# Kernel tuning notes

Hardware: AMD Instinct MI355X
Metric: run time of the kernel (lower is better)

## Reference

```python
import jax, jax.numpy as jnp
import numpy as np

ALPHA = 0.2   # leaky relu negative slope
NEG_INF = -1e12


def setup_inputs() -> dict:
    key = jax.random.key(0)
    k1, k2, k3, k4 = jax.random.split(key, 4)
    B, N, H = 8, 2048, 128
    inp = jax.random.normal(k1, (B, N, H), dtype=jnp.float32)
    A = (jax.random.uniform(k2, (B, N, N)) < 0.05).astype(jnp.float32)
    # xavier_uniform with gain 1.414
    gain = 1.414
    limW = gain * np.sqrt(6.0 / (H + H))
    W = jax.random.uniform(k3, (H, H), minval=-limW, maxval=limW, dtype=jnp.float32)
    lima = gain * np.sqrt(6.0 / (2 * H + 1))
    a = jax.random.uniform(k4, (2 * H, 1), minval=-lima, maxval=lima, dtype=jnp.float32)
    return {"inp": inp, "A": A, "W": W, "a": a}


def reference(inp, A, W, a):
    B, N, H = inp.shape
    Wh = jnp.matmul(inp, W)                      # [B,N,H]
    Wh1 = jnp.matmul(Wh, a[:H, :])               # [B,N,1]
    Wh2 = jnp.matmul(Wh, a[H:, :])               # [B,N,1]
    A_ = A + jnp.eye(N, dtype=A.dtype)           # add self loops
    e = (Wh1 + jnp.swapaxes(Wh2, 1, 2)) * A_     # [B,N,N]
    e = jnp.where(e >= 0, e, ALPHA * e)          # leaky relu
    scores = jnp.where(A_ > 0, e, NEG_INF)
    attention = jax.nn.softmax(scores, axis=2)   # dropout: eval mode -> identity
    h_prime = jnp.matmul(attention, Wh)          # [B,N,H]
    return jax.nn.elu(h_prime)                   # concat=True branch
```

## Files before the change

kernel.cpp:

```cpp
#include <hip/hip_runtime.h>
#include <hip/hip_bf16.h>
#include <math.h>

typedef __attribute__((ext_vector_type(4))) float f32x4;
typedef __attribute__((ext_vector_type(8))) short s16x8;

constexpr int Nc = 2048;
constexpr int Hc = 128;
constexpr int ROWS = 8 * 2048;

__device__ __forceinline__ unsigned short f2bf(float f) {
  unsigned u = __float_as_uint(f);
  return (unsigned short)((u + 0x7fffu + ((u >> 16) & 1u)) >> 16);
}
__device__ __forceinline__ float bf2f(unsigned short b) {
  return __uint_as_float(((unsigned)b) << 16);
}

typedef __attribute__((address_space(3))) unsigned u32_lds;
typedef __attribute__((address_space(1))) const unsigned u32_glb;
__device__ __forceinline__ void stage16(const void* g, void* l) {
  __builtin_amdgcn_global_load_lds((u32_glb*)g, (u32_lds*)l, 16, 0, 0);
}

__global__ void prep_kernel(const float* __restrict__ W,
                            unsigned short* __restrict__ Wt_hi,
                            unsigned short* __restrict__ Wt_lo) {
  const int id = blockIdx.x * 256 + threadIdx.x;
  const int k = id >> 7, h = id & 127;
  const float w = W[id];
  const unsigned short hi = f2bf(w);
  const unsigned short lo = f2bf(w - bf2f(hi));
  const int off = ((k >> 3) * 128 + h) * 8 + (k & 7);
  Wt_hi[off] = hi;
  Wt_lo[off] = lo;
}

__global__ __launch_bounds__(256) void whmfma_kernel(
    const float* __restrict__ inp, const unsigned short* __restrict__ Wt_hi,
    const unsigned short* __restrict__ Wt_lo, const float* __restrict__ a,
    unsigned short* __restrict__ Vsw, float* __restrict__ Wh1,
    float* __restrict__ Wh2) {
  const int t = threadIdx.x, w_ = t >> 6, l = t & 63;
  const int lrow = l & 15, kq = l >> 4;
  const int r0 = blockIdx.x * 64 + w_ * 16;
  const int row = r0 + lrow;

  s16x8 ahi[4], alo[4];
#pragma unroll
  for (int ks = 0; ks < 4; ++ks) {
    const float* xp = inp + (size_t)row * 128 + ks * 32 + kq * 8;
    const f32x4 x0 = *(const f32x4*)xp;
    const f32x4 x1 = *(const f32x4*)(xp + 4);
    s16x8 th, tl;
#pragma unroll
    for (int e = 0; e < 4; ++e) {
      const unsigned short b0 = f2bf(x0[e]), b1 = f2bf(x1[e]);
      th[e] = (short)b0;       tl[e] = (short)f2bf(x0[e] - bf2f(b0));
      th[4 + e] = (short)b1;   tl[4 + e] = (short)f2bf(x1[e] - bf2f(b1));
    }
    ahi[ks] = th; alo[ks] = tl;
  }

  f32x4 acc[8];
#pragma unroll
  for (int nb = 0; nb < 8; ++nb) acc[nb] = (f32x4){0.f, 0.f, 0.f, 0.f};

#pragma unroll
  for (int ks = 0; ks < 4; ++ks) {
#pragma unroll
    for (int nb = 0; nb < 8; ++nb) {
      const size_t bo = ((size_t)(ks * 4 + kq) * 128 + nb * 16 + lrow) * 8;
      const s16x8 bh = *(const s16x8*)(Wt_hi + bo);
      const s16x8 bl = *(const s16x8*)(Wt_lo + bo);
      acc[nb] = __builtin_amdgcn_mfma_f32_16x16x32_bf16(ahi[ks], bh, acc[nb], 0, 0, 0);
      acc[nb] = __builtin_amdgcn_mfma_f32_16x16x32_bf16(alo[ks], bh, acc[nb], 0, 0, 0);
      acc[nb] = __builtin_amdgcn_mfma_f32_16x16x32_bf16(ahi[ks], bl, acc[nb], 0, 0, 0);
    }
  }

  float a1v[8], a2v[8];
#pragma unroll
  for (int nb = 0; nb < 8; ++nb) {
    a1v[nb] = a[nb * 16 + lrow];
    a2v[nb] = a[128 + nb * 16 + lrow];
  }
#pragma unroll
  for (int rg = 0; rg < 4; ++rg) {
    float p1 = 0.f, p2 = 0.f;
#pragma unroll
    for (int nb = 0; nb < 8; ++nb) {
      p1 = fmaf(acc[nb][rg], a1v[nb], p1);
      p2 = fmaf(acc[nb][rg], a2v[nb], p2);
    }
#pragma unroll
    for (int off = 1; off < 16; off <<= 1) {
      p1 += __shfl_xor(p1, off);
      p2 += __shfl_xor(p2, off);
    }
    if (lrow == 0) {
      const int node = r0 + kq * 4 + rg;
      Wh1[node] = p1;
      Wh2[node] = p2;
    }
  }

  const int b = r0 >> 11, jt = (r0 >> 6) & 31;
  unsigned short* __restrict__ vbase = Vsw + (size_t)(b * 32 + jt) * (8 * 128 * 8);
  const int nl0 = w_ * 16 + kq * 4;
  const int jg = nl0 >> 3, j0 = nl0 & 7;
#pragma unroll
  for (int nb = 0; nb < 8; ++nb) {
    unsigned q0, q1;
    asm("v_cvt_pk_bf16_f32 %0, %1, %2" : "=v"(q0) : "v"(acc[nb][0]), "v"(acc[nb][1]));
    asm("v_cvt_pk_bf16_f32 %0, %1, %2" : "=v"(q1) : "v"(acc[nb][2]), "v"(acc[nb][3]));
    *(uint2*)(vbase + ((size_t)jg * 128 + nb * 16 + lrow) * 8 + j0) = make_uint2(q0, q1);
  }
}

__global__ __launch_bounds__(256, 3) void attn_kernel(
    const float* __restrict__ A, const unsigned short* __restrict__ Vsw,
    const float* __restrict__ Wh1, const float* __restrict__ Wh2,
    float* __restrict__ out) {
  __shared__ union {
    struct { float Ab[2][16][256]; float w2[2][256]; } st;
    struct { float m[64]; float l[64]; float invl[16]; float a4[4][16][132]; } mg;
  } sm;

  const int t = threadIdx.x, w_ = t >> 6, l = t & 63;
  const int lrow = l & 15, lq = l >> 4, g8 = lq * 8;
  const int bid = (blockIdx.x & 7) * 128 + (blockIdx.x >> 3);
  const int b = bid >> 7;
  const int irow = (bid & 127) * 16 + lrow;

  const float* __restrict__ Abase = A + (size_t)bid * 16 * 2048;
  const float* __restrict__ Wh2b = Wh2 + (size_t)b * 2048;
  const float wh1r = Wh1[(size_t)bid * 16 + lrow];
  const unsigned short* __restrict__ Vb = Vsw + (size_t)b * (32 * 8 * 128 * 8);
  const size_t vlane = (size_t)(lq * 128 + lrow) * 8;

#pragma unroll
  for (int rr = 0; rr < 4; ++rr) {
    const int r = w_ * 4 + rr;
    stage16(Abase + (size_t)r * 2048 + ((l ^ (r & 7)) << 2), &sm.st.Ab[0][r][0]);
  }
  if (w_ == 0) stage16(Wh2b + l * 4, &sm.st.w2[0][0]);

  f32x4 acc[8];
#pragma unroll
  for (int nb = 0; nb < 8; ++nb) acc[nb] = (f32x4){0.f, 0.f, 0.f, 0.f};
  float m = -1e30f, lsum = 0.f;

  for (int c = 0; c < 8; ++c) {
    __syncthreads();
    const int buf = c & 1;
    if (c < 7) {
#pragma unroll
      for (int rr = 0; rr < 4; ++rr) {
        const int r = w_ * 4 + rr;
        stage16(Abase + (size_t)r * 2048 + (c + 1) * 256 + ((l ^ (r & 7)) << 2),
                &sm.st.Ab[buf ^ 1][r][0]);
      }
      if (w_ == 0) stage16(Wh2b + (c + 1) * 256 + l * 4, &sm.st.w2[buf ^ 1][0]);
    }

    const int jb_loc = w_ * 64;
    const int jb_glob = c * 256 + jb_loc;
    const unsigned short* __restrict__ Vt = Vb + (size_t)(c * 4 + w_) * (8 * 128 * 8);

    s16x8 v0[4], v1[4];
#pragma unroll
    for (int nb = 0; nb < 4; ++nb) {
      v0[nb] = *(const s16x8*)(Vt + vlane + nb * 128);
      v1[nb] = *(const s16x8*)(Vt + vlane + 4096 + nb * 128);
    }

    f32x4 av[4], wv[4];
    const int c0 = (jb_loc + g8) >> 2;
#pragma unroll
    for (int q = 0; q < 4; ++q) {
      const int cq = c0 + (q & 1) + (q >> 1) * 8;
      av[q] = *(const f32x4*)&sm.st.Ab[buf][lrow][(cq ^ (lrow & 7)) << 2];
      wv[q] = *(const f32x4*)&sm.st.w2[buf][jb_loc + g8 + (q & 1) * 4 + (q >> 1) * 32];
    }

    float s[16];
    float tm = -3e30f;
#pragma unroll
    for (int idx = 0; idx < 16; ++idx) {
      const int j = jb_glob + (idx >> 3) * 32 + g8 + (idx & 7);
      const float aval = av[idx >> 2][idx & 3];
      const float raw = wh1r + wv[idx >> 2][idx & 3];
      const float lr = fmaxf(raw, 0.2f * raw);
      const float mult = aval + ((j == irow) ? 1.f : 0.f);
      const float sv = (mult > 0.f) ? mult * lr : -2e30f;
      s[idx] = sv;
      tm = fmaxf(tm, sv);
    }
    tm = fmaxf(tm, __shfl_xor(tm, 16));
    tm = fmaxf(tm, __shfl_xor(tm, 32));
    const float mnew = (tm > m + 8.f) ? tm : m;
    if (__ballot(mnew != m)) {
      const float alpha = __expf(m - mnew);
      lsum *= alpha;
      const int rb4 = lq * 4;
      const float a0 = __shfl(alpha, rb4);
      const float a1 = __shfl(alpha, rb4 + 1);
      const float a2 = __shfl(alpha, rb4 + 2);
      const float a3 = __shfl(alpha, rb4 + 3);
#pragma unroll
      for (int nb = 0; nb < 8; ++nb) {
        acc[nb][0] *= a0; acc[nb][1] *= a1; acc[nb][2] *= a2; acc[nb][3] *= a3;
      }
      m = mnew;
    }

    float p[16];
    float tsum = 0.f;
#pragma unroll
    for (int idx = 0; idx < 16; ++idx) {
      p[idx] = __expf(s[idx] - m);
      tsum += p[idx];
    }
    tsum += __shfl_xor(tsum, 16);
    tsum += __shfl_xor(tsum, 32);
    lsum += tsum;

    union { unsigned u[4]; s16x8 v; } pk0, pk1;
#pragma unroll
    for (int q = 0; q < 4; ++q) {
      asm("v_cvt_pk_bf16_f32 %0, %1, %2" : "=v"(pk0.u[q]) : "v"(p[2 * q]), "v"(p[2 * q + 1]));
      asm("v_cvt_pk_bf16_f32 %0, %1, %2" : "=v"(pk1.u[q]) : "v"(p[8 + 2 * q]), "v"(p[9 + 2 * q]));
    }

    s16x8 v2[4], v3[4];
#pragma unroll
    for (int nb = 0; nb < 4; ++nb) {
      v2[nb] = *(const s16x8*)(Vt + vlane + (nb + 4) * 128);
      v3[nb] = *(const s16x8*)(Vt + vlane + 4096 + (nb + 4) * 128);
    }
#pragma unroll
    for (int nb = 0; nb < 4; ++nb) {
      acc[nb] = __builtin_amdgcn_mfma_f32_16x16x32_bf16(pk0.v, v0[nb], acc[nb], 0, 0, 0);
      acc[nb] = __builtin_amdgcn_mfma_f32_16x16x32_bf16(pk1.v, v1[nb], acc[nb], 0, 0, 0);
    }
#pragma unroll
    for (int nb = 0; nb < 4; ++nb) {
      acc[nb + 4] = __builtin_amdgcn_mfma_f32_16x16x32_bf16(pk0.v, v2[nb], acc[nb + 4], 0, 0, 0);
      acc[nb + 4] = __builtin_amdgcn_mfma_f32_16x16x32_bf16(pk1.v, v3[nb], acc[nb + 4], 0, 0, 0);
    }
  }

  __syncthreads();
  if (l < 16) { sm.mg.m[w_ * 16 + l] = m; sm.mg.l[w_ * 16 + l] = lsum; }
  __syncthreads();

  if (t < 16) {
    const float m0 = sm.mg.m[t], m1 = sm.mg.m[16 + t];
    const float m2 = sm.mg.m[32 + t], m3 = sm.mg.m[48 + t];
    const float ms = fmaxf(fmaxf(m0, m1), fmaxf(m2, m3));
    const float ls = sm.mg.l[t] * __expf(m0 - ms) + sm.mg.l[16 + t] * __expf(m1 - ms)
                   + sm.mg.l[32 + t] * __expf(m2 - ms) + sm.mg.l[48 + t] * __expf(m3 - ms);
    sm.mg.invl[t] = 1.f / ls;
  }
  float beta[4];
#pragma unroll
  for (int rg = 0; rg < 4; ++rg) {
    const int rd = lq * 4 + rg;
    const float m0 = sm.mg.m[rd], m1 = sm.mg.m[16 + rd];
    const float m2 = sm.mg.m[32 + rd], m3 = sm.mg.m[48 + rd];
    const float ms = fmaxf(fmaxf(m0, m1), fmaxf(m2, m3));
    beta[rg] = __expf(sm.mg.m[w_ * 16 + rd] - ms);
  }
#pragma unroll
  for (int nb = 0; nb < 8; ++nb)
#pragma unroll
    for (int rg = 0; rg < 4; ++rg)
      sm.mg.a4[w_][lq * 4 + rg][nb * 16 + lrow] = acc[nb][rg] * beta[rg];
  __syncthreads();

  const int h = w_ * 32 + (l & 31);
  float* __restrict__ outp = out + (size_t)bid * 16 * 128;
#pragma unroll
  for (int i = 0; i < 8; ++i) {
    const int r = (l >> 5) + 2 * i;
    float v = (sm.mg.a4[0][r][h] + sm.mg.a4[1][r][h] +
               sm.mg.a4[2][r][h] + sm.mg.a4[3][r][h]) * sm.mg.invl[r];
    outp[(size_t)r * 128 + h] = (v > 0.f) ? v : expm1f(v);
  }
}

extern "C" void kernel_launch(void* const* d_in, const int* in_sizes, int n_in,
                              void* d_out, int out_size, void* d_ws, size_t ws_size,
                              hipStream_t stream) {
  const float* inp = (const float*)d_in[0];
  const float* A   = (const float*)d_in[1];
  const float* W   = (const float*)d_in[2];
  const float* a   = (const float*)d_in[3];
  float* out = (float*)d_out;

  char* ws = (char*)d_ws;
  unsigned short* Vsw = (unsigned short*)ws;  ws += (size_t)8 * 32 * 8 * 128 * 8 * 2;
  float* Wh1 = (float*)ws;                    ws += (size_t)ROWS * 4;
  float* Wh2 = (float*)ws;                    ws += (size_t)ROWS * 4;
  unsigned short* Wt_hi = (unsigned short*)ws; ws += 128 * 128 * 2;
  unsigned short* Wt_lo = (unsigned short*)ws; ws += 128 * 128 * 2;

  prep_kernel<<<dim3(64), dim3(256), 0, stream>>>(W, Wt_hi, Wt_lo);
  whmfma_kernel<<<dim3(256), dim3(256), 0, stream>>>(inp, Wt_hi, Wt_lo, a, Vsw, Wh1, Wh2);
  attn_kernel<<<dim3(1024), dim3(256), 0, stream>>>(A, Vsw, Wh1, Wh2, out);
}
```

Baseline: 228.4 us.

## Use precomputed per-batch score upper bound to drop online softmax rescaling

Adds a per-batch max reduction of Wh2 and uses leakyrelu(Wh1+max Wh2), times a factor of 2 to cover the self-loop multiplier, as a fixed softmax shift. The online max tracking, rescaling and cross-wave merge are no longer needed. The attention A-tile staging becomes a three-buffer pipeline with one barrier per chunk, and Wh2 is read directly from global memory. The Wh projection kernel now stages W and the input in LDS with smaller blocks. The fixed shift risks underflow of exp when a row's true max is far below the bound, and it adds one extra kernel launch.

```diff
diff --git a/kernel.cpp b/kernel.cpp
--- a/kernel.cpp
+++ b/kernel.cpp
@@ -5,8 +5,6 @@
 typedef __attribute__((ext_vector_type(4))) float f32x4;
 typedef __attribute__((ext_vector_type(8))) short s16x8;
 
-constexpr int Nc = 2048;
-constexpr int Hc = 128;
 constexpr int ROWS = 8 * 2048;
 
 __device__ __forceinline__ unsigned short f2bf(float f) {
@@ -36,22 +34,45 @@
   Wt_lo[off] = lo;
 }
 
-__global__ __launch_bounds__(256) void whmfma_kernel(
+__global__ __launch_bounds__(128, 2) void whmfma_kernel(
     const float* __restrict__ inp, const unsigned short* __restrict__ Wt_hi,
     const unsigned short* __restrict__ Wt_lo, const float* __restrict__ a,
     unsigned short* __restrict__ Vsw, float* __restrict__ Wh1,
     float* __restrict__ Wh2) {
+  __shared__ unsigned short WtH[16][128][8];
+  __shared__ unsigned short WtL[16][128][8];
+  __shared__ float xl[32][128];
+
   const int t = threadIdx.x, w_ = t >> 6, l = t & 63;
   const int lrow = l & 15, kq = l >> 4;
-  const int r0 = blockIdx.x * 64 + w_ * 16;
-  const int row = r0 + lrow;
+  const int rbase = blockIdx.x * 32;
+  const int r0 = rbase + w_ * 16;
+
+#pragma unroll
+  for (int i = 0; i < 16; ++i) {
+    stage16(Wt_hi + (size_t)(i * 128 + w_ * 64 + l) * 8,
+            &WtH[0][0][0] + (size_t)(i * 128 + w_ * 64) * 8);
+    stage16(Wt_lo + (size_t)(i * 128 + w_ * 64 + l) * 8,
+            &WtL[0][0][0] + (size_t)(i * 128 + w_ * 64) * 8);
+  }
+#pragma unroll
+  for (int s = 0; s < 8; ++s) {
+    const int rloc = w_ * 16 + 2 * s + (l >> 5);
+    stage16(inp + (size_t)(rbase + rloc) * 128 + (((l & 31) ^ (rloc & 7)) << 2),
+            &xl[w_ * 16 + 2 * s][0]);
+  }
+  asm volatile("s_waitcnt vmcnt(0)" ::: "memory");
+  __builtin_amdgcn_sched_barrier(0);
+  __syncthreads();
+  __builtin_amdgcn_sched_barrier(0);
 
   s16x8 ahi[4], alo[4];
 #pragma unroll
   for (int ks = 0; ks < 4; ++ks) {
-    const float* xp = inp + (size_t)row * 128 + ks * 32 + kq * 8;
-    const f32x4 x0 = *(const f32x4*)xp;
-    const f32x4 x1 = *(const f32x4*)(xp + 4);
+    const int g0 = ks * 8 + kq * 2;
+    const int sw = lrow & 7;
+    const f32x4 x0 = *(const f32x4*)&xl[w_ * 16 + lrow][(g0 ^ sw) << 2];
+    const f32x4 x1 = *(const f32x4*)&xl[w_ * 16 + lrow][((g0 + 1) ^ sw) << 2];
     s16x8 th, tl;
 #pragma unroll
     for (int e = 0; e < 4; ++e) {
@@ -70,9 +91,8 @@
   for (int ks = 0; ks < 4; ++ks) {
 #pragma unroll
     for (int nb = 0; nb < 8; ++nb) {
-      const size_t bo = ((size_t)(ks * 4 + kq) * 128 + nb * 16 + lrow) * 8;
-      const s16x8 bh = *(const s16x8*)(Wt_hi + bo);
-      const s16x8 bl = *(const s16x8*)(Wt_lo + bo);
+      const s16x8 bh = *(const s16x8*)&WtH[ks * 4 + kq][nb * 16 + lrow][0];
+      const s16x8 bl = *(const s16x8*)&WtL[ks * 4 + kq][nb * 16 + lrow][0];
       acc[nb] = __builtin_amdgcn_mfma_f32_16x16x32_bf16(ahi[ks], bh, acc[nb], 0, 0, 0);
       acc[nb] = __builtin_amdgcn_mfma_f32_16x16x32_bf16(alo[ks], bh, acc[nb], 0, 0, 0);
       acc[nb] = __builtin_amdgcn_mfma_f32_16x16x32_bf16(ahi[ks], bl, acc[nb], 0, 0, 0);
@@ -99,16 +119,15 @@
       p2 += __shfl_xor(p2, off);
     }
     if (lrow == 0) {
-      const int node = r0 + kq * 4 + rg;
-      Wh1[node] = p1;
-      Wh2[node] = p2;
-    }
-  }
-
-  const int b = r0 >> 11, jt = (r0 >> 6) & 31;
+      Wh1[r0 + kq * 4 + rg] = p1;
+      Wh2[r0 + kq * 4 + rg] = p2;
+    }
+  }
+
+  const int row_g = r0 + kq * 4;
+  const int b = row_g >> 11, jt = (row_g >> 6) & 31;
+  const int nl0 = row_g & 63, jg = nl0 >> 3, j0 = nl0 & 7;
   unsigned short* __restrict__ vbase = Vsw + (size_t)(b * 32 + jt) * (8 * 128 * 8);
-  const int nl0 = w_ * 16 + kq * 4;
-  const int jg = nl0 >> 3, j0 = nl0 & 7;
 #pragma unroll
   for (int nb = 0; nb < 8; ++nb) {
     unsigned q0, q1;
@@ -118,13 +137,27 @@
   }
 }
 
+__global__ void maxred_kernel(const float* __restrict__ Wh2, float* __restrict__ Mh2) {
+  __shared__ float ls[4];
+  const int b = blockIdx.x, t = threadIdx.x;
+  const f32x4* p = (const f32x4*)(Wh2 + (size_t)b * 2048);
+  const f32x4 v0 = p[t], v1 = p[t + 256];
+  float m = fmaxf(fmaxf(fmaxf(v0[0], v0[1]), fmaxf(v0[2], v0[3])),
+                  fmaxf(fmaxf(v1[0], v1[1]), fmaxf(v1[2], v1[3])));
+#pragma unroll
+  for (int off = 1; off < 64; off <<= 1) m = fmaxf(m, __shfl_xor(m, off));
+  if ((t & 63) == 0) ls[t >> 6] = m;
+  __syncthreads();
+  if (t == 0) Mh2[b] = fmaxf(fmaxf(ls[0], ls[1]), fmaxf(ls[2], ls[3]));
+}
+
 __global__ __launch_bounds__(256, 3) void attn_kernel(
     const float* __restrict__ A, const unsigned short* __restrict__ Vsw,
     const float* __restrict__ Wh1, const float* __restrict__ Wh2,
-    float* __restrict__ out) {
+    const float* __restrict__ Mh2, float* __restrict__ out) {
   __shared__ union {
-    struct { float Ab[2][16][256]; float w2[2][256]; } st;
-    struct { float m[64]; float l[64]; float invl[16]; float a4[4][16][132]; } mg;
+    float Ab[3][16][256];
+    struct { float l[64]; float invl[16]; float a4[4][16][132]; } mg;
   } sm;
 
   const int t = threadIdx.x, w_ = t >> 6, l = t & 63;
@@ -139,31 +172,26 @@
   const unsigned short* __restrict__ Vb = Vsw + (size_t)b * (32 * 8 * 128 * 8);
   const size_t vlane = (size_t)(lq * 128 + lrow) * 8;
 
-#pragma unroll
-  for (int rr = 0; rr < 4; ++rr) {
-    const int r = w_ * 4 + rr;
-    stage16(Abase + (size_t)r * 2048 + ((l ^ (r & 7)) << 2), &sm.st.Ab[0][r][0]);
-  }
-  if (w_ == 0) stage16(Wh2b + l * 4, &sm.st.w2[0][0]);
+  const float rawu = wh1r + Mh2[b];
+  const float lru = fmaxf(rawu, 0.2f * rawu);
+  const float m = fmaxf(2.f * lru, lru);
+
+#pragma unroll
+  for (int cc = 0; cc < 2; ++cc)
+#pragma unroll
+    for (int rr = 0; rr < 4; ++rr) {
+      const int r = w_ * 4 + rr;
+      stage16(Abase + (size_t)r * 2048 + cc * 256 + ((l ^ (r & 7)) << 2),
+              &sm.Ab[cc][r][0]);
+    }
 
   f32x4 acc[8];
 #pragma unroll
   for (int nb = 0; nb < 8; ++nb) acc[nb] = (f32x4){0.f, 0.f, 0.f, 0.f};
-  float m = -1e30f, lsum = 0.f;
+  float lsum = 0.f;
 
   for (int c = 0; c < 8; ++c) {
-    __syncthreads();
-    const int buf = c & 1;
-    if (c < 7) {
-#pragma unroll
-      for (int rr = 0; rr < 4; ++rr) {
-        const int r = w_ * 4 + rr;
-        stage16(Abase + (size_t)r * 2048 + (c + 1) * 256 + ((l ^ (r & 7)) << 2),
-                &sm.st.Ab[buf ^ 1][r][0]);
-      }
-      if (w_ == 0) stage16(Wh2b + (c + 1) * 256 + l * 4, &sm.st.w2[buf ^ 1][0]);
-    }
-
+    const int buf = c % 3;
     const int jb_loc = w_ * 64;
     const int jb_glob = c * 256 + jb_loc;
     const unsigned short* __restrict__ Vt = Vb + (size_t)(c * 4 + w_) * (8 * 128 * 8);
@@ -174,18 +202,34 @@
       v0[nb] = *(const s16x8*)(Vt + vlane + nb * 128);
       v1[nb] = *(const s16x8*)(Vt + vlane + 4096 + nb * 128);
     }
-
-    f32x4 av[4], wv[4];
+    f32x4 wv[4];
+#pragma unroll
+    for (int q = 0; q < 4; ++q)
+      wv[q] = *(const f32x4*)(Wh2b + jb_glob + g8 + (q & 1) * 4 + (q >> 1) * 32);
+
+    asm volatile("s_waitcnt vmcnt(16)" ::: "memory");
+    __builtin_amdgcn_sched_barrier(0);
+    __builtin_amdgcn_s_barrier();
+    __builtin_amdgcn_sched_barrier(0);
+
+    if (c < 6) {
+#pragma unroll
+      for (int rr = 0; rr < 4; ++rr) {
+        const int r = w_ * 4 + rr;
+        stage16(Abase + (size_t)r * 2048 + (c + 2) * 256 + ((l ^ (r & 7)) << 2),
+                &sm.Ab[(c + 2) % 3][r][0]);
+      }
+    }
+
+    f32x4 av[4];
     const int c0 = (jb_loc + g8) >> 2;
 #pragma unroll
     for (int q = 0; q < 4; ++q) {
       const int cq = c0 + (q & 1) + (q >> 1) * 8;
-      av[q] = *(const f32x4*)&sm.st.Ab[buf][lrow][(cq ^ (lrow & 7)) << 2];
-      wv[q] = *(const f32x4*)&sm.st.w2[buf][jb_loc + g8 + (q & 1) * 4 + (q >> 1) * 32];
-    }
-
-    float s[16];
-    float tm = -3e30f;
+      av[q] = *(const f32x4*)&sm.Ab[buf][lrow][(cq ^ (lrow & 7)) << 2];
+    }
+
+    float p[16];
 #pragma unroll
     for (int idx = 0; idx < 16; ++idx) {
       const int j = jb_glob + (idx >> 3) * 32 + g8 + (idx & 7);
@@ -193,38 +237,9 @@
       const float raw = wh1r + wv[idx >> 2][idx & 3];
       const float lr = fmaxf(raw, 0.2f * raw);
       const float mult = aval + ((j == irow) ? 1.f : 0.f);
-      const float sv = (mult > 0.f) ? mult * lr : -2e30f;
-      s[idx] = sv;
-      tm = fmaxf(tm, sv);
-    }
-    tm = fmaxf(tm, __shfl_xor(tm, 16));
-    tm = fmaxf(tm, __shfl_xor(tm, 32));
-    const float mnew = (tm > m + 8.f) ? tm : m;
-    if (__ballot(mnew != m)) {
-      const float alpha = __expf(m - mnew);
-      lsum *= alpha;
-      const int rb4 = lq * 4;
-      const float a0 = __shfl(alpha, rb4);
-      const float a1 = __shfl(alpha, rb4 + 1);
-      const float a2 = __shfl(alpha, rb4 + 2);
-      const float a3 = __shfl(alpha, rb4 + 3);
-#pragma unroll
-      for (int nb = 0; nb < 8; ++nb) {
-        acc[nb][0] *= a0; acc[nb][1] *= a1; acc[nb][2] *= a2; acc[nb][3] *= a3;
-      }
-      m = mnew;
-    }
-
-    float p[16];
-    float tsum = 0.f;
-#pragma unroll
-    for (int idx = 0; idx < 16; ++idx) {
-      p[idx] = __expf(s[idx] - m);
-      tsum += p[idx];
-    }
-    tsum += __shfl_xor(tsum, 16);
-    tsum += __shfl_xor(tsum, 32);
-    lsum += tsum;
+      p[idx] = (mult > 0.f) ? __expf(mult * lr - m) : 0.f;
+      lsum += p[idx];
+    }
 
     union { unsigned u[4]; s16x8 v; } pk0, pk1;
 #pragma unroll
@@ -251,32 +266,18 @@
     }
   }
 
-  __syncthreads();
-  if (l < 16) { sm.mg.m[w_ * 16 + l] = m; sm.mg.l[w_ * 16 + l] = lsum; }
-  __syncthreads();
-
-  if (t < 16) {
-    const float m0 = sm.mg.m[t], m1 = sm.mg.m[16 + t];
-    const float m2 = sm.mg.m[32 + t], m3 = sm.mg.m[48 + t];
-    const float ms = fmaxf(fmaxf(m0, m1), fmaxf(m2, m3));
-    const float ls = sm.mg.l[t] * __expf(m0 - ms) + sm.mg.l[16 + t] * __expf(m1 - ms)
-                   + sm.mg.l[32 + t] * __expf(m2 - ms) + sm.mg.l[48 + t] * __expf(m3 - ms);
-    sm.mg.invl[t] = 1.f / ls;
-  }
-  float beta[4];
-#pragma unroll
-  for (int rg = 0; rg < 4; ++rg) {
-    const int rd = lq * 4 + rg;
-    const float m0 = sm.mg.m[rd], m1 = sm.mg.m[16 + rd];
-    const float m2 = sm.mg.m[32 + rd], m3 = sm.mg.m[48 + rd];
-    const float ms = fmaxf(fmaxf(m0, m1), fmaxf(m2, m3));
-    beta[rg] = __expf(sm.mg.m[w_ * 16 + rd] - ms);
-  }
+  lsum += __shfl_xor(lsum, 16);
+  lsum += __shfl_xor(lsum, 32);
+  __syncthreads();
+  if (l < 16) sm.mg.l[w_ * 16 + l] = lsum;
+  __syncthreads();
+  if (t < 16)
+    sm.mg.invl[t] = 1.f / (sm.mg.l[t] + sm.mg.l[16 + t] + sm.mg.l[32 + t] + sm.mg.l[48 + t]);
 #pragma unroll
   for (int nb = 0; nb < 8; ++nb)
 #pragma unroll
     for (int rg = 0; rg < 4; ++rg)
-      sm.mg.a4[w_][lq * 4 + rg][nb * 16 + lrow] = acc[nb][rg] * beta[rg];
+      sm.mg.a4[w_][lq * 4 + rg][nb * 16 + lrow] = acc[nb][rg];
   __syncthreads();
 
   const int h = w_ * 32 + (l & 31);
@@ -300,13 +301,15 @@
   float* out = (float*)d_out;
 
   char* ws = (char*)d_ws;
-  unsigned short* Vsw = (unsigned short*)ws;  ws += (size_t)8 * 32 * 8 * 128 * 8 * 2;
-  float* Wh1 = (float*)ws;                    ws += (size_t)ROWS * 4;
-  float* Wh2 = (float*)ws;                    ws += (size_t)ROWS * 4;
+  unsigned short* Vsw = (unsigned short*)ws;   ws += (size_t)8 * 32 * 8 * 128 * 8 * 2;
+  float* Wh1 = (float*)ws;                     ws += (size_t)ROWS * 4;
+  float* Wh2 = (float*)ws;                     ws += (size_t)ROWS * 4;
   unsigned short* Wt_hi = (unsigned short*)ws; ws += 128 * 128 * 2;
   unsigned short* Wt_lo = (unsigned short*)ws; ws += 128 * 128 * 2;
+  float* Mh2 = (float*)ws;                     ws += 8 * 4;
 
   prep_kernel<<<dim3(64), dim3(256), 0, stream>>>(W, Wt_hi, Wt_lo);
-  whmfma_kernel<<<dim3(256), dim3(256), 0, stream>>>(inp, Wt_hi, Wt_lo, a, Vsw, Wh1, Wh2);
-  attn_kernel<<<dim3(1024), dim3(256), 0, stream>>>(A, Vsw, Wh1, Wh2, out);
-}
+  whmfma_kernel<<<dim3(512), dim3(128), 0, stream>>>(inp, Wt_hi, Wt_lo, a, Vsw, Wh1, Wh2);
+  maxred_kernel<<<dim3(8), dim3(256), 0, stream>>>(Wh2, Mh2);
+  attn_kernel<<<dim3(1024), dim3(256), 0, stream>>>(A, Vsw, Wh1, Wh2, Mh2, out);
+}
```

After: 231.6 us. No clear change (+1.4%).
